# Optimization experiments

Measured on AMD Instinct MI355X. Metric: run time of the kernel, lower is better.

## Reference

```python
import jax, jax.numpy as jnp
import numpy as np

N_NODES = 20000
N_EDGES = 160000
IN_F = 128
HID_HEADS, HID_CH = 32, 32
OUT_EMB = 64
NEG_SLOPE = 0.2


def setup_inputs() -> dict:
    key = jax.random.key(0)
    ks = jax.random.split(key, 8)
    x = jax.random.normal(ks[0], (N_NODES, IN_F), dtype=jnp.float32)
    edge_index = jax.random.randint(ks[1], (2, N_EDGES), 0, N_NODES, dtype=jnp.int32)
    W1 = jax.random.normal(ks[2], (IN_F, HID_HEADS * HID_CH), dtype=jnp.float32) / np.sqrt(IN_F)
    att_src1 = jax.random.normal(ks[3], (HID_HEADS, HID_CH), dtype=jnp.float32) / np.sqrt(HID_CH)
    att_dst1 = jax.random.normal(ks[4], (HID_HEADS, HID_CH), dtype=jnp.float32) / np.sqrt(HID_CH)
    b1 = jnp.zeros((HID_HEADS * HID_CH,), dtype=jnp.float32)
    W2 = jax.random.normal(ks[5], (HID_HEADS * HID_CH, OUT_EMB), dtype=jnp.float32) / np.sqrt(HID_HEADS * HID_CH)
    att_src2 = jax.random.normal(ks[6], (1, OUT_EMB), dtype=jnp.float32) / np.sqrt(OUT_EMB)
    att_dst2 = jax.random.normal(ks[7], (1, OUT_EMB), dtype=jnp.float32) / np.sqrt(OUT_EMB)
    b2 = jnp.zeros((OUT_EMB,), dtype=jnp.float32)
    return {"x": x, "edge_index": edge_index, "W1": W1, "att_src1": att_src1,
            "att_dst1": att_dst1, "b1": b1, "W2": W2, "att_src2": att_src2,
            "att_dst2": att_dst2, "b2": b2}


def _gat_conv(x, src, dst, W, a_src, a_dst, b, n_nodes):
    # PyG GATConv (eval mode): per-head linear, edge attention, segment softmax over
    # incoming edges of each target node, weighted scatter-sum, concat heads + bias.
    H, C = a_src.shape
    h = (x @ W).reshape(-1, H, C)                       # [N, H, C]
    e_s = jnp.einsum('nhc,hc->nh', h, a_src)            # [N, H]
    e_d = jnp.einsum('nhc,hc->nh', h, a_dst)            # [N, H]
    e = jax.nn.leaky_relu(e_s[src] + e_d[dst], NEG_SLOPE)  # [E, H]
    m = jax.ops.segment_max(e, dst, num_segments=n_nodes)  # [N, H]
    m = jnp.where(jnp.isfinite(m), m, jnp.zeros_like(m))   # nodes w/o in-edges
    ex = jnp.exp(e - m[dst])                            # [E, H]
    s = jax.ops.segment_sum(ex, dst, num_segments=n_nodes)
    alpha = ex / (s[dst] + 1e-16)                       # [E, H]
    msg = h[src] * alpha[:, :, None]                    # [E, H, C]
    out = jax.ops.segment_sum(msg, dst, num_segments=n_nodes)  # [N, H, C]
    return out.reshape(n_nodes, H * C) + b


def reference(x, edge_index, W1, att_src1, att_dst1, b1, W2, att_src2, att_dst2, b2):
    n = x.shape[0]
    loops = jnp.arange(n, dtype=edge_index.dtype)
    src = jnp.concatenate([edge_index[0], loops])  # PyG adds self-loops by default
    dst = jnp.concatenate([edge_index[1], loops])
    h = jax.nn.elu(_gat_conv(x, src, dst, W1, att_src1, att_dst1, b1, n))
    out = _gat_conv(h, src, dst, W2, att_src2, att_dst2, b2, n)
    return out
```

## Files before the change

kernel.cpp:

```cpp
#include <hip/hip_runtime.h>
#include <hip/hip_bf16.h>
#include <math.h>

typedef __attribute__((ext_vector_type(8))) short bf16x8;
typedef __attribute__((ext_vector_type(4))) float f32x4;
typedef __attribute__((ext_vector_type(8))) unsigned short u16x8;

__device__ inline float bf2f(unsigned short u) {
    union { float f; unsigned int i; } c; c.i = ((unsigned int)u) << 16; return c.f;
}
__device__ inline unsigned short f2bf(float f) {
    union { float f; unsigned int i; } c; c.f = f;
    unsigned int r = c.i + 0x7fffu + ((c.i >> 16) & 1u);
    return (unsigned short)(r >> 16);
}

__global__ void cast_f32_bf16(const float* __restrict__ in, unsigned short* __restrict__ out,
                              int count4) {
    int i = blockIdx.x * blockDim.x + threadIdx.x;
    if (i >= count4) return;
    float4 v = *(const float4*)&in[(size_t)i * 4];
    ushort4 o;
    o.x = f2bf(v.x); o.y = f2bf(v.y); o.z = f2bf(v.z); o.w = f2bf(v.w);
    *(ushort4*)&out[(size_t)i * 4] = o;
}

__global__ void transpose_cast(const float* __restrict__ W, unsigned short* __restrict__ WT,
                               int K, int N) {
    int idx = blockIdx.x * blockDim.x + threadIdx.x;
    if (idx >= K * N) return;
    int nn = idx / K, kk = idx - nn * K;
    WT[idx] = f2bf(W[(size_t)kk * N + nn]);
}

__global__ __launch_bounds__(256) void gemm_mfma_attn(const unsigned short* __restrict__ A,
                                                      const unsigned short* __restrict__ BT,
                                                      unsigned short* __restrict__ C,
                                                      const float* __restrict__ asrc,
                                                      const float* __restrict__ adst,
                                                      float* __restrict__ es,
                                                      float* __restrict__ ed,
                                                      int M, int N, int K) {
    int tid = threadIdx.x;
    int wid = tid >> 6, lane = tid & 63;
    int wm = wid >> 1, wn = wid & 1;
    int m0 = blockIdx.x * 64 + wm * 32;
    int n0 = blockIdx.y * 64 + wn * 32;
    int lr = lane & 15;
    int q  = lane >> 4;
    int lk = q * 8;

    int ra0 = min(m0 + lr, M - 1);
    int ra1 = min(m0 + 16 + lr, M - 1);
    const unsigned short* pa0 = A + (size_t)ra0 * K + lk;
    const unsigned short* pa1 = A + (size_t)ra1 * K + lk;
    const unsigned short* pb0 = BT + (size_t)(n0 + lr) * K + lk;
    const unsigned short* pb1 = BT + (size_t)(n0 + 16 + lr) * K + lk;

    f32x4 acc00 = {0,0,0,0}, acc01 = {0,0,0,0}, acc10 = {0,0,0,0}, acc11 = {0,0,0,0};
    for (int k = 0; k < K; k += 64) {
        bf16x8 a0 = *(const bf16x8*)(pa0 + k);
        bf16x8 a1 = *(const bf16x8*)(pa1 + k);
        bf16x8 b0 = *(const bf16x8*)(pb0 + k);
        bf16x8 b1 = *(const bf16x8*)(pb1 + k);
        bf16x8 a0b = *(const bf16x8*)(pa0 + k + 32);
        bf16x8 a1b = *(const bf16x8*)(pa1 + k + 32);
        bf16x8 b0b = *(const bf16x8*)(pb0 + k + 32);
        bf16x8 b1b = *(const bf16x8*)(pb1 + k + 32);
        acc00 = __builtin_amdgcn_mfma_f32_16x16x32_bf16(a0, b0, acc00, 0, 0, 0);
        acc01 = __builtin_amdgcn_mfma_f32_16x16x32_bf16(a0, b1, acc01, 0, 0, 0);
        acc10 = __builtin_amdgcn_mfma_f32_16x16x32_bf16(a1, b0, acc10, 0, 0, 0);
        acc11 = __builtin_amdgcn_mfma_f32_16x16x32_bf16(a1, b1, acc11, 0, 0, 0);
        acc00 = __builtin_amdgcn_mfma_f32_16x16x32_bf16(a0b, b0b, acc00, 0, 0, 0);
        acc01 = __builtin_amdgcn_mfma_f32_16x16x32_bf16(a0b, b1b, acc01, 0, 0, 0);
        acc10 = __builtin_amdgcn_mfma_f32_16x16x32_bf16(a1b, b0b, acc10, 0, 0, 0);
        acc11 = __builtin_amdgcn_mfma_f32_16x16x32_bf16(a1b, b1b, acc11, 0, 0, 0);
    }
    int srow = q * 4;
    #pragma unroll
    for (int r = 0; r < 4; ++r) {
        int r0 = m0 + srow + r, r1 = m0 + 16 + srow + r;
        if (r0 < M) {
            C[(size_t)r0 * N + n0 + lr]      = f2bf(acc00[r]);
            C[(size_t)r0 * N + n0 + 16 + lr] = f2bf(acc01[r]);
        }
        if (r1 < M) {
            C[(size_t)r1 * N + n0 + lr]      = f2bf(acc10[r]);
            C[(size_t)r1 * N + n0 + 16 + lr] = f2bf(acc11[r]);
        }
    }
    int head = blockIdx.y * 2 + wn;
    float as_lo = asrc[head * 32 + lr], as_hi = asrc[head * 32 + 16 + lr];
    float ad_lo = adst[head * 32 + lr], ad_hi = adst[head * 32 + 16 + lr];
    #pragma unroll
    for (int X = 0; X < 2; ++X) {
        f32x4 ac0 = X ? acc10 : acc00;
        f32x4 ac1 = X ? acc11 : acc01;
        #pragma unroll
        for (int r = 0; r < 4; ++r) {
            float ps = ac0[r] * as_lo + ac1[r] * as_hi;
            float pd = ac0[r] * ad_lo + ac1[r] * ad_hi;
            #pragma unroll
            for (int msk = 1; msk < 16; msk <<= 1) {
                ps += __shfl_xor(ps, msk);
                pd += __shfl_xor(pd, msk);
            }
            int row = m0 + X * 16 + q * 4 + r;
            if (lr == 0 && row < M) {
                es[row * 32 + head] = ps;
                ed[row * 32 + head] = pd;
            }
        }
    }
}

__global__ __launch_bounds__(256) void gemm_mfma(const unsigned short* __restrict__ A,
                                                 const unsigned short* __restrict__ BT,
                                                 unsigned short* __restrict__ C,
                                                 int M, int N, int K) {
    int tid = threadIdx.x;
    int wid = tid >> 6, lane = tid & 63;
    int wm = wid >> 1, wn = wid & 1;
    int m0 = blockIdx.x * 64 + wm * 32;
    int n0 = blockIdx.y * 64 + wn * 32;
    int lr = lane & 15;
    int lk = (lane >> 4) * 8;

    int ra0 = min(m0 + lr, M - 1);
    int ra1 = min(m0 + 16 + lr, M - 1);
    const unsigned short* pa0 = A + (size_t)ra0 * K + lk;
    const unsigned short* pa1 = A + (size_t)ra1 * K + lk;
    const unsigned short* pb0 = BT + (size_t)(n0 + lr) * K + lk;
    const unsigned short* pb1 = BT + (size_t)(n0 + 16 + lr) * K + lk;

    f32x4 acc00 = {0,0,0,0}, acc01 = {0,0,0,0}, acc10 = {0,0,0,0}, acc11 = {0,0,0,0};
    for (int k = 0; k < K; k += 64) {
        bf16x8 a0 = *(const bf16x8*)(pa0 + k);
        bf16x8 a1 = *(const bf16x8*)(pa1 + k);
        bf16x8 b0 = *(const bf16x8*)(pb0 + k);
        bf16x8 b1 = *(const bf16x8*)(pb1 + k);
        bf16x8 a0b = *(const bf16x8*)(pa0 + k + 32);
        bf16x8 a1b = *(const bf16x8*)(pa1 + k + 32);
        bf16x8 b0b = *(const bf16x8*)(pb0 + k + 32);
        bf16x8 b1b = *(const bf16x8*)(pb1 + k + 32);
        acc00 = __builtin_amdgcn_mfma_f32_16x16x32_bf16(a0, b0, acc00, 0, 0, 0);
        acc01 = __builtin_amdgcn_mfma_f32_16x16x32_bf16(a0, b1, acc01, 0, 0, 0);
        acc10 = __builtin_amdgcn_mfma_f32_16x16x32_bf16(a1, b0, acc10, 0, 0, 0);
        acc11 = __builtin_amdgcn_mfma_f32_16x16x32_bf16(a1, b1, acc11, 0, 0, 0);
        acc00 = __builtin_amdgcn_mfma_f32_16x16x32_bf16(a0b, b0b, acc00, 0, 0, 0);
        acc01 = __builtin_amdgcn_mfma_f32_16x16x32_bf16(a0b, b1b, acc01, 0, 0, 0);
        acc10 = __builtin_amdgcn_mfma_f32_16x16x32_bf16(a1b, b0b, acc10, 0, 0, 0);
        acc11 = __builtin_amdgcn_mfma_f32_16x16x32_bf16(a1b, b1b, acc11, 0, 0, 0);
    }
    int srow = (lane >> 4) * 4;
    #pragma unroll
    for (int r = 0; r < 4; ++r) {
        int r0 = m0 + srow + r, r1 = m0 + 16 + srow + r;
        if (r0 < M) {
            C[(size_t)r0 * N + n0 + lr]      = f2bf(acc00[r]);
            C[(size_t)r0 * N + n0 + 16 + lr] = f2bf(acc01[r]);
        }
        if (r1 < M) {
            C[(size_t)r1 * N + n0 + lr]      = f2bf(acc10[r]);
            C[(size_t)r1 * N + n0 + 16 + lr] = f2bf(acc11[r]);
        }
    }
}

__global__ void count_edges(const int* __restrict__ ei, int* __restrict__ counts,
                            int E0, int n) {
    int e = blockIdx.x * blockDim.x + threadIdx.x;
    int Etot = E0 + n;
    if (e >= Etot) return;
    int dst = (e < E0) ? ei[E0 + e] : (e - E0);
    atomicAdd(&counts[dst], 1);
}

__global__ void scan_excl(const int* __restrict__ counts, int* __restrict__ offsets, int n) {
    __shared__ int wpre[16];
    __shared__ int total_s;
    __shared__ int running_s;
    int tid = threadIdx.x, lane = tid & 63, w = tid >> 6;
    if (tid == 0) running_s = 0;
    __syncthreads();
    for (int base = 0; base < n; base += 1024) {
        int i = base + tid;
        int v = (i < n) ? counts[i] : 0;
        int incl = v;
        #pragma unroll
        for (int d = 1; d < 64; d <<= 1) {
            int t = __shfl_up(incl, d);
            if (lane >= d) incl += t;
        }
        if (lane == 63) wpre[w] = incl;
        __syncthreads();
        if (w == 0) {
            int s = (lane < 16) ? wpre[lane] : 0;
            int sc = s;
            #pragma unroll
            for (int d = 1; d < 16; d <<= 1) {
                int t = __shfl_up(sc, d);
                if (lane >= d) sc += t;
            }
            if (lane < 16) wpre[lane] = sc - s;
            if (lane == 15) total_s = sc;
        }
        __syncthreads();
        int r = running_s;
        if (i < n) offsets[i] = r + wpre[w] + incl - v;
        __syncthreads();
        if (tid == 0) running_s = r + total_s;
        __syncthreads();
    }
    if (tid == 0) offsets[n] = running_s;
}

__global__ void fill_edges(const int* __restrict__ ei, const int* __restrict__ offsets,
                           int* __restrict__ cursor, int* __restrict__ srcs,
                           int E0, int n) {
    int e = blockIdx.x * blockDim.x + threadIdx.x;
    int Etot = E0 + n;
    if (e >= Etot) return;
    int src, dst;
    if (e < E0) { src = ei[e]; dst = ei[E0 + e]; }
    else        { src = dst = e - E0; }
    int pos = offsets[dst] + atomicAdd(&cursor[dst], 1);
    srcs[pos] = src;
}

__global__ __launch_bounds__(256) void stats1(const float* __restrict__ es,
                                              const float* __restrict__ ed,
                                              const int* __restrict__ offsets,
                                              const int* __restrict__ srcs,
                                              float* __restrict__ et,
                                              float* __restrict__ sinv, int n) {
    int node = blockIdx.x;
    int tid = threadIdx.x;
    int h2 = tid & 31, j2 = tid >> 5;
    __shared__ float sed[32];
    __shared__ float red[4][32];
    int beg = offsets[node], end = offsets[node + 1];
    if (tid < 32) sed[tid] = ed[node * 32 + tid];
    __syncthreads();
    float edh = sed[h2];
    float ssum = 0.f;
    for (int e = beg + j2; e < end; e += 8) {
        int s = srcs[e];
        float ev = es[s * 32 + h2] + edh;
        ev = ev > 0.f ? ev : 0.2f * ev;
        float t = __expf(ev);
        et[(size_t)e * 32 + h2] = t;
        ssum += t;
    }
    ssum += __shfl_xor(ssum, 32);
    int w = tid >> 6;
    if ((tid & 63) < 32) red[w][h2] = ssum;
    __syncthreads();
    if (tid < 32) {
        float s = red[0][tid] + red[1][tid] + red[2][tid] + red[3][tid];
        sinv[node * 32 + tid] = 1.0f / (s + 1e-16f);
    }
}

__global__ __launch_bounds__(256) void gather1(const unsigned short* __restrict__ hb,
                                               const float* __restrict__ et,
                                               const float* __restrict__ sinv,
                                               const int* __restrict__ offsets,
                                               const int* __restrict__ srcs,
                                               const float* __restrict__ b1,
                                               unsigned short* __restrict__ out, int n) {
    int node = blockIdx.x;
    int tid = threadIdx.x;
    int ep = tid >> 7;
    int t2 = tid & 127;
    int head = t2 >> 2;
    int c8 = (t2 & 3) * 8;
    int hoff = head * 32 + c8;
    int beg = offsets[node], end = offsets[node + 1];
    float a[8] = {0.f,0.f,0.f,0.f,0.f,0.f,0.f,0.f};
    int e = beg + ep;
    for (; e + 2 < end; e += 4) {
        int s0 = srcs[e], s1 = srcs[e + 2];
        float t0 = et[(size_t)e * 32 + head];
        float t1 = et[(size_t)(e + 2) * 32 + head];
        u16x8 h0 = *(const u16x8*)&hb[(size_t)s0 * 1024 + hoff];
        u16x8 h1 = *(const u16x8*)&hb[(size_t)s1 * 1024 + hoff];
        #pragma unroll
        for (int j = 0; j < 8; ++j) a[j] += t0 * bf2f(h0[j]) + t1 * bf2f(h1[j]);
    }
    if (e < end) {
        int s0 = srcs[e];
        float t0 = et[(size_t)e * 32 + head];
        u16x8 h0 = *(const u16x8*)&hb[(size_t)s0 * 1024 + hoff];
        #pragma unroll
        for (int j = 0; j < 8; ++j) a[j] += t0 * bf2f(h0[j]);
    }
    __shared__ float lds[128][9];
    if (ep == 1) {
        #pragma unroll
        for (int j = 0; j < 8; ++j) lds[t2][j] = a[j];
    }
    __syncthreads();
    if (ep == 0) {
        float si = sinv[node * 32 + head];
        float4 bl = *(const float4*)&b1[hoff];
        float4 bh = *(const float4*)&b1[hoff + 4];
        float bb[8] = {bl.x, bl.y, bl.z, bl.w, bh.x, bh.y, bh.z, bh.w};
        u16x8 o8;
        #pragma unroll
        for (int j = 0; j < 8; ++j) {
            float r = (a[j] + lds[t2][j]) * si + bb[j];
            r = r > 0.f ? r : expm1f(r);
            o8[j] = f2bf(r);
        }
        *(u16x8*)&out[(size_t)node * 1024 + hoff] = o8;
    }
}

__global__ void attn_scores2(const unsigned short* __restrict__ hb2,
                             const float* __restrict__ asrc,
                             const float* __restrict__ adst,
                             float* __restrict__ es, float* __restrict__ ed, int n) {
    int node = blockIdx.x * (blockDim.x >> 6) + (threadIdx.x >> 6);
    int lane = threadIdx.x & 63;
    if (node >= n) return;
    float v = bf2f(hb2[(size_t)node * 64 + lane]);
    float s1 = v * asrc[lane];
    float s2 = v * adst[lane];
    #pragma unroll
    for (int o = 1; o < 64; o <<= 1) {
        s1 += __shfl_xor(s1, o);
        s2 += __shfl_xor(s2, o);
    }
    if (lane == 0) { es[node] = s1; ed[node] = s2; }
}

__global__ void stats2(const float* __restrict__ es, const float* __restrict__ ed,
                       const int* __restrict__ offsets, const int* __restrict__ srcs,
                       float* __restrict__ et2, float* __restrict__ sinv2, int n) {
    int node = blockIdx.x * (blockDim.x >> 6) + (threadIdx.x >> 6);
    int lane = threadIdx.x & 63;
    if (node >= n) return;
    int beg = offsets[node], end = offsets[node + 1];
    float edv = ed[node];
    float ssum = 0.f;
    for (int e = beg + lane; e < end; e += 64) {
        float ev = es[srcs[e]] + edv;
        ev = ev > 0.f ? ev : 0.2f * ev;
        float t = __expf(ev);
        et2[e] = t;
        ssum += t;
    }
    #pragma unroll
    for (int o = 1; o < 64; o <<= 1) ssum += __shfl_xor(ssum, o);
    if (lane == 0) sinv2[node] = 1.0f / (ssum + 1e-16f);
}

__global__ void gather2(const unsigned short* __restrict__ hb2,
                        const float* __restrict__ et2,
                        const float* __restrict__ sinv2,
                        const int* __restrict__ offsets, const int* __restrict__ srcs,
                        const float* __restrict__ b2, float* __restrict__ out, int n) {
    int node = blockIdx.x * (blockDim.x >> 6) + (threadIdx.x >> 6);
    int lane = threadIdx.x & 63;
    if (node >= n) return;
    int beg = offsets[node], end = offsets[node + 1];
    float acc = 0.f;
    int e = beg;
    for (; e + 1 < end; e += 2) {
        int s0 = srcs[e], s1 = srcs[e + 1];
        float t0 = et2[e], t1 = et2[e + 1];
        acc += t0 * bf2f(hb2[(size_t)s0 * 64 + lane])
             + t1 * bf2f(hb2[(size_t)s1 * 64 + lane]);
    }
    if (e < end) {
        acc += et2[e] * bf2f(hb2[(size_t)srcs[e] * 64 + lane]);
    }
    out[(size_t)node * 64 + lane] = acc * sinv2[node] + b2[lane];
}

extern "C" void kernel_launch(void* const* d_in, const int* in_sizes, int n_in,
                              void* d_out, int out_size, void* d_ws, size_t ws_size,
                              hipStream_t stream) {
    const float* x        = (const float*)d_in[0];
    const int*   ei       = (const int*)d_in[1];
    const float* W1       = (const float*)d_in[2];
    const float* att_src1 = (const float*)d_in[3];
    const float* att_dst1 = (const float*)d_in[4];
    const float* b1       = (const float*)d_in[5];
    const float* W2       = (const float*)d_in[6];
    const float* att_src2 = (const float*)d_in[7];
    const float* att_dst2 = (const float*)d_in[8];
    const float* b2       = (const float*)d_in[9];
    float* out = (float*)d_out;

    int n  = in_sizes[0] / 128;
    int E0 = in_sizes[1] / 2;
    int Etot = E0 + n;

    float* ws = (float*)d_ws;
    size_t off = 0;
    unsigned short* hb1 = (unsigned short*)(ws + off); off += (size_t)n * 512;
    unsigned short* hact = (unsigned short*)(ws + off); off += (size_t)n * 512;
    unsigned short* hb2 = (unsigned short*)(ws + off); off += (size_t)n * 32;
    unsigned short* xb  = (unsigned short*)(ws + off); off += (size_t)n * 64;
    unsigned short* W1T = (unsigned short*)(ws + off); off += 1024 * 128 / 2;
    unsigned short* W2T = (unsigned short*)(ws + off); off += 64 * 1024 / 2;
    float* es1  = ws + off; off += (size_t)n * 32;
    float* ed1  = ws + off; off += (size_t)n * 32;
    float* et1  = ws + off; off += (size_t)Etot * 32;
    float* sinv1 = ws + off; off += (size_t)n * 32;
    float* et2  = ws + off; off += (size_t)Etot;
    float* sinv2 = ws + off; off += (size_t)n;
    int* counts  = (int*)(ws + off); off += n;
    int* cursor  = (int*)(ws + off); off += n;
    int* offsets = (int*)(ws + off); off += n + 8;
    int* srcs    = (int*)(ws + off); off += Etot;
    float* es2 = es1;
    float* ed2 = ed1;

    cast_f32_bf16<<<(n * 128 / 4 + 255) / 256, 256, 0, stream>>>(x, xb, n * 128 / 4);
    transpose_cast<<<(128 * 1024 + 255) / 256, 256, 0, stream>>>(W1, W1T, 128, 1024);
    transpose_cast<<<(1024 * 64 + 255) / 256, 256, 0, stream>>>(W2, W2T, 1024, 64);

    hipMemsetAsync(counts, 0, 2 * (size_t)n * sizeof(int), stream);
    count_edges<<<(Etot + 255) / 256, 256, 0, stream>>>(ei, counts, E0, n);
    scan_excl<<<1, 1024, 0, stream>>>(counts, offsets, n);
    fill_edges<<<(Etot + 255) / 256, 256, 0, stream>>>(ei, offsets, cursor, srcs, E0, n);

    gemm_mfma_attn<<<dim3((n + 63) / 64, 1024 / 64), 256, 0, stream>>>(
        xb, W1T, hb1, att_src1, att_dst1, es1, ed1, n, 1024, 128);
    stats1<<<n, 256, 0, stream>>>(es1, ed1, offsets, srcs, et1, sinv1, n);
    gather1<<<n, 256, 0, stream>>>(hb1, et1, sinv1, offsets, srcs, b1, hact, n);

    gemm_mfma<<<dim3((n + 63) / 64, 64 / 64), 256, 0, stream>>>(hact, W2T, hb2, n, 64, 1024);
    attn_scores2<<<(n + 3) / 4, 256, 0, stream>>>(hb2, att_src2, att_dst2, es2, ed2, n);
    stats2<<<(n + 3) / 4, 256, 0, stream>>>(es2, ed2, offsets, srcs, et2, sinv2, n);
    gather2<<<(n + 3) / 4, 256, 0, stream>>>(hb2, et2, sinv2, offsets, srcs, b2, out, n);
}
```

Baseline: 238.1 us.

## Fuse layer-2 GEMM with attention scores using split-K across waves

Replaces the second-layer GEMM with a kernel that processes 32 rows per block, splits K=1024 across four waves, and reduces the partial sums through shared memory. The attention source and destination dot products are computed in the epilogue, so the separate attn_scores2 kernel and its reread of hb2 are no longer needed. This change also unrolls the gather2 edge loop by four to keep more loads in flight. The grid assumes n is a multiple of 32 and drops row bounds checks. It also uses 32KB of shared memory per block, which may limit occupancy.

```diff
diff --git a/kernel.cpp b/kernel.cpp
--- a/kernel.cpp
+++ b/kernel.cpp
@@ -114,57 +114,87 @@
     }
 }
 
-__global__ __launch_bounds__(256) void gemm_mfma(const unsigned short* __restrict__ A,
-                                                 const unsigned short* __restrict__ BT,
-                                                 unsigned short* __restrict__ C,
-                                                 int M, int N, int K) {
-    int tid = threadIdx.x;
-    int wid = tid >> 6, lane = tid & 63;
-    int wm = wid >> 1, wn = wid & 1;
-    int m0 = blockIdx.x * 64 + wm * 32;
-    int n0 = blockIdx.y * 64 + wn * 32;
-    int lr = lane & 15;
-    int lk = (lane >> 4) * 8;
-
-    int ra0 = min(m0 + lr, M - 1);
-    int ra1 = min(m0 + 16 + lr, M - 1);
-    const unsigned short* pa0 = A + (size_t)ra0 * K + lk;
-    const unsigned short* pa1 = A + (size_t)ra1 * K + lk;
-    const unsigned short* pb0 = BT + (size_t)(n0 + lr) * K + lk;
-    const unsigned short* pb1 = BT + (size_t)(n0 + 16 + lr) * K + lk;
-
-    f32x4 acc00 = {0,0,0,0}, acc01 = {0,0,0,0}, acc10 = {0,0,0,0}, acc11 = {0,0,0,0};
-    for (int k = 0; k < K; k += 64) {
-        bf16x8 a0 = *(const bf16x8*)(pa0 + k);
-        bf16x8 a1 = *(const bf16x8*)(pa1 + k);
-        bf16x8 b0 = *(const bf16x8*)(pb0 + k);
-        bf16x8 b1 = *(const bf16x8*)(pb1 + k);
+__global__ __launch_bounds__(256) void gemm2_fused(const unsigned short* __restrict__ A,
+                                                   const unsigned short* __restrict__ BT,
+                                                   unsigned short* __restrict__ C,
+                                                   const float* __restrict__ asrc,
+                                                   const float* __restrict__ adst,
+                                                   float* __restrict__ es,
+                                                   float* __restrict__ ed, int M) {
+    const int K = 1024;
+    int tid = threadIdx.x, wid = tid >> 6, lane = tid & 63;
+    int m0 = blockIdx.x * 32;
+    int lr = lane & 15, q = lane >> 4, lk = q * 8;
+    int k0 = wid * 256;
+
+    const unsigned short* pa0 = A + (size_t)(m0 + lr) * K + k0 + lk;
+    const unsigned short* pa1 = A + (size_t)(m0 + 16 + lr) * K + k0 + lk;
+    const unsigned short* pb0 = BT + (size_t)(0  + lr) * K + k0 + lk;
+    const unsigned short* pb1 = BT + (size_t)(16 + lr) * K + k0 + lk;
+    const unsigned short* pb2 = BT + (size_t)(32 + lr) * K + k0 + lk;
+    const unsigned short* pb3 = BT + (size_t)(48 + lr) * K + k0 + lk;
+
+    f32x4 acc[2][4] = {};
+    for (int k = 0; k < 256; k += 64) {
+        bf16x8 a0  = *(const bf16x8*)(pa0 + k);
+        bf16x8 a1  = *(const bf16x8*)(pa1 + k);
         bf16x8 a0b = *(const bf16x8*)(pa0 + k + 32);
         bf16x8 a1b = *(const bf16x8*)(pa1 + k + 32);
+        bf16x8 b0  = *(const bf16x8*)(pb0 + k);
         bf16x8 b0b = *(const bf16x8*)(pb0 + k + 32);
+        acc[0][0] = __builtin_amdgcn_mfma_f32_16x16x32_bf16(a0,  b0,  acc[0][0], 0, 0, 0);
+        acc[1][0] = __builtin_amdgcn_mfma_f32_16x16x32_bf16(a1,  b0,  acc[1][0], 0, 0, 0);
+        acc[0][0] = __builtin_amdgcn_mfma_f32_16x16x32_bf16(a0b, b0b, acc[0][0], 0, 0, 0);
+        acc[1][0] = __builtin_amdgcn_mfma_f32_16x16x32_bf16(a1b, b0b, acc[1][0], 0, 0, 0);
+        bf16x8 b1  = *(const bf16x8*)(pb1 + k);
         bf16x8 b1b = *(const bf16x8*)(pb1 + k + 32);
-        acc00 = __builtin_amdgcn_mfma_f32_16x16x32_bf16(a0, b0, acc00, 0, 0, 0);
-        acc01 = __builtin_amdgcn_mfma_f32_16x16x32_bf16(a0, b1, acc01, 0, 0, 0);
-        acc10 = __builtin_amdgcn_mfma_f32_16x16x32_bf16(a1, b0, acc10, 0, 0, 0);
-        acc11 = __builtin_amdgcn_mfma_f32_16x16x32_bf16(a1, b1, acc11, 0, 0, 0);
-        acc00 = __builtin_amdgcn_mfma_f32_16x16x32_bf16(a0b, b0b, acc00, 0, 0, 0);
-        acc01 = __builtin_amdgcn_mfma_f32_16x16x32_bf16(a0b, b1b, acc01, 0, 0, 0);
-        acc10 = __builtin_amdgcn_mfma_f32_16x16x32_bf16(a1b, b0b, acc10, 0, 0, 0);
-        acc11 = __builtin_amdgcn_mfma_f32_16x16x32_bf16(a1b, b1b, acc11, 0, 0, 0);
-    }
-    int srow = (lane >> 4) * 4;
-    #pragma unroll
-    for (int r = 0; r < 4; ++r) {
-        int r0 = m0 + srow + r, r1 = m0 + 16 + srow + r;
-        if (r0 < M) {
-            C[(size_t)r0 * N + n0 + lr]      = f2bf(acc00[r]);
-            C[(size_t)r0 * N + n0 + 16 + lr] = f2bf(acc01[r]);
-        }
-        if (r1 < M) {
-            C[(size_t)r1 * N + n0 + lr]      = f2bf(acc10[r]);
-            C[(size_t)r1 * N + n0 + 16 + lr] = f2bf(acc11[r]);
-        }
-    }
+        acc[0][1] = __builtin_amdgcn_mfma_f32_16x16x32_bf16(a0,  b1,  acc[0][1], 0, 0, 0);
+        acc[1][1] = __builtin_amdgcn_mfma_f32_16x16x32_bf16(a1,  b1,  acc[1][1], 0, 0, 0);
+        acc[0][1] = __builtin_amdgcn_mfma_f32_16x16x32_bf16(a0b, b1b, acc[0][1], 0, 0, 0);
+        acc[1][1] = __builtin_amdgcn_mfma_f32_16x16x32_bf16(a1b, b1b, acc[1][1], 0, 0, 0);
+        bf16x8 b2  = *(const bf16x8*)(pb2 + k);
+        bf16x8 b2b = *(const bf16x8*)(pb2 + k + 32);
+        acc[0][2] = __builtin_amdgcn_mfma_f32_16x16x32_bf16(a0,  b2,  acc[0][2], 0, 0, 0);
+        acc[1][2] = __builtin_amdgcn_mfma_f32_16x16x32_bf16(a1,  b2,  acc[1][2], 0, 0, 0);
+        acc[0][2] = __builtin_amdgcn_mfma_f32_16x16x32_bf16(a0b, b2b, acc[0][2], 0, 0, 0);
+        acc[1][2] = __builtin_amdgcn_mfma_f32_16x16x32_bf16(a1b, b2b, acc[1][2], 0, 0, 0);
+        bf16x8 b3  = *(const bf16x8*)(pb3 + k);
+        bf16x8 b3b = *(const bf16x8*)(pb3 + k + 32);
+        acc[0][3] = __builtin_amdgcn_mfma_f32_16x16x32_bf16(a0,  b3,  acc[0][3], 0, 0, 0);
+        acc[1][3] = __builtin_amdgcn_mfma_f32_16x16x32_bf16(a1,  b3,  acc[1][3], 0, 0, 0);
+        acc[0][3] = __builtin_amdgcn_mfma_f32_16x16x32_bf16(a0b, b3b, acc[0][3], 0, 0, 0);
+        acc[1][3] = __builtin_amdgcn_mfma_f32_16x16x32_bf16(a1b, b3b, acc[1][3], 0, 0, 0);
+    }
+    __shared__ float red[4][32][64];
+    #pragma unroll
+    for (int rf = 0; rf < 2; ++rf)
+        #pragma unroll
+        for (int cf = 0; cf < 4; ++cf)
+            #pragma unroll
+            for (int i = 0; i < 4; ++i)
+                red[wid][rf * 16 + q * 4 + i][cf * 16 + lr] = acc[rf][cf][i];
+    __syncthreads();
+    int r = tid >> 3, c0 = (tid & 7) * 8;
+    float v[8];
+    #pragma unroll
+    for (int j = 0; j < 8; ++j)
+        v[j] = red[0][r][c0 + j] + red[1][r][c0 + j] + red[2][r][c0 + j] + red[3][r][c0 + j];
+    u16x8 o8;
+    float ps = 0.f, pd = 0.f;
+    #pragma unroll
+    for (int j = 0; j < 8; ++j) {
+        o8[j] = f2bf(v[j]);
+        ps += v[j] * asrc[c0 + j];
+        pd += v[j] * adst[c0 + j];
+    }
+    int row = m0 + r;
+    *(u16x8*)&C[(size_t)row * 64 + c0] = o8;
+    #pragma unroll
+    for (int msk = 1; msk < 8; msk <<= 1) {
+        ps += __shfl_xor(ps, msk);
+        pd += __shfl_xor(pd, msk);
+    }
+    if ((tid & 7) == 0) { es[row] = ps; ed[row] = pd; }
 }
 
 __global__ void count_edges(const int* __restrict__ ei, int* __restrict__ counts,
@@ -317,24 +347,6 @@
     }
 }
 
-__global__ void attn_scores2(const unsigned short* __restrict__ hb2,
-                             const float* __restrict__ asrc,
-                             const float* __restrict__ adst,
-                             float* __restrict__ es, float* __restrict__ ed, int n) {
-    int node = blockIdx.x * (blockDim.x >> 6) + (threadIdx.x >> 6);
-    int lane = threadIdx.x & 63;
-    if (node >= n) return;
-    float v = bf2f(hb2[(size_t)node * 64 + lane]);
-    float s1 = v * asrc[lane];
-    float s2 = v * adst[lane];
-    #pragma unroll
-    for (int o = 1; o < 64; o <<= 1) {
-        s1 += __shfl_xor(s1, o);
-        s2 += __shfl_xor(s2, o);
-    }
-    if (lane == 0) { es[node] = s1; ed[node] = s2; }
-}
-
 __global__ void stats2(const float* __restrict__ es, const float* __restrict__ ed,
                        const int* __restrict__ offsets, const int* __restrict__ srcs,
                        float* __restrict__ et2, float* __restrict__ sinv2, int n) {
@@ -367,13 +379,15 @@
     int beg = offsets[node], end = offsets[node + 1];
     float acc = 0.f;
     int e = beg;
-    for (; e + 1 < end; e += 2) {
-        int s0 = srcs[e], s1 = srcs[e + 1];
-        float t0 = et2[e], t1 = et2[e + 1];
+    for (; e + 3 < end; e += 4) {
+        int s0 = srcs[e], s1 = srcs[e + 1], s2 = srcs[e + 2], s3 = srcs[e + 3];
+        float t0 = et2[e], t1 = et2[e + 1], t2 = et2[e + 2], t3 = et2[e + 3];
         acc += t0 * bf2f(hb2[(size_t)s0 * 64 + lane])
-             + t1 * bf2f(hb2[(size_t)s1 * 64 + lane]);
-    }
-    if (e < end) {
+             + t1 * bf2f(hb2[(size_t)s1 * 64 + lane])
+             + t2 * bf2f(hb2[(size_t)s2 * 64 + lane])
+             + t3 * bf2f(hb2[(size_t)s3 * 64 + lane]);
+    }
+    for (; e < end; ++e) {
         acc += et2[e] * bf2f(hb2[(size_t)srcs[e] * 64 + lane]);
     }
     out[(size_t)node * 64 + lane] = acc * sinv2[node] + b2[lane];
@@ -433,8 +447,7 @@
     stats1<<<n, 256, 0, stream>>>(es1, ed1, offsets, srcs, et1, sinv1, n);
     gather1<<<n, 256, 0, stream>>>(hb1, et1, sinv1, offsets, srcs, b1, hact, n);
 
-    gemm_mfma<<<dim3((n + 63) / 64, 64 / 64), 256, 0, stream>>>(hact, W2T, hb2, n, 64, 1024);
-    attn_scores2<<<(n + 3) / 4, 256, 0, stream>>>(hb2, att_src2, att_dst2, es2, ed2, n);
+    gemm2_fused<<<n / 32, 256, 0, stream>>>(hact, W2T, hb2, att_src2, att_dst2, es2, ed2, n);
     stats2<<<(n + 3) / 4, 256, 0, stream>>>(es2, ed2, offsets, srcs, et2, sinv2, n);
     gather2<<<(n + 3) / 4, 256, 0, stream>>>(hb2, et2, sinv2, offsets, srcs, b2, out, n);
 }
```

Measured after the change: 219.2 us. -7.9%, faster.
